# Kernel tuning notes

Measured on AMD Instinct MI355X. Metric: run time of the kernel, lower is better.

Reference implementation:

```python
import jax, jax.numpy as jnp
import numpy as np

N_FREQ = 256
VOCAB = 50257
N_CHANNELS = 1024
B, S = 4, 1024


def setup_inputs() -> dict:
    key = jax.random.key(0)
    k1, k2 = jax.random.split(key)
    h = jax.random.normal(k1, (B, S, N_CHANNELS), dtype=jnp.float32)
    weight = jax.random.normal(k2, (N_CHANNELS, 2 * N_FREQ), dtype=jnp.float32) * 0.02
    return {"h": h, "weight": weight}


def reference(h, weight):
    n = N_FREQ
    V = VOCAB
    # channel -> frequency coefficients (real part then imag part)
    Y_ri = h.astype(jnp.float32) @ weight  # [B, S, 2n]
    Y = jax.lax.complex(Y_ri[..., :n], Y_ri[..., n:])  # [B, S, n]
    # zero-padded half-spectrum: bins 1..n carry Y, DC and high bins are zero
    full = jnp.zeros(h.shape[:-1] + (V // 2 + 1,), dtype=jnp.complex64)
    full = full.at[..., 1:n + 1].set(Y)
    out = jnp.fft.irfft(full, n=V, axis=-1)  # [B, S, V]
    return out.astype(h.dtype)
```

## Files before the change

### kernel.cpp

```cpp
#include <hip/hip_runtime.h>
#include <hip/hip_fp16.h>
#include <stdint.h>

#define V_N   50257
#define NPAN  393
#define NCH   1024
#define MT    4096
#define KC    512
#define NFRQ  256
#define TWO_PI 6.28318530717958647692f

typedef _Float16 f16;
typedef __attribute__((ext_vector_type(8))) _Float16 f16x8;
typedef __attribute__((ext_vector_type(4))) float    f32x4;

__device__ __forceinline__ void gload_lds16(const void* g, const void* l) {
  typedef const __attribute__((address_space(1))) unsigned int* gp_t;
  typedef __attribute__((address_space(3))) unsigned int* lp_t;
  __builtin_amdgcn_global_load_lds((gp_t)(uint64_t)(uintptr_t)g,
                                   (lp_t)(uint32_t)(uintptr_t)l, 16, 0, 0);
}

__global__ __launch_bounds__(256) void k1_proj(
    const float* __restrict__ h, const float* __restrict__ w, f16* __restrict__ A) {
  __shared__ __align__(16) f16 As[64 * 64];
  __shared__ __align__(16) f16 Bs[64 * 64];
  const int tid = threadIdx.x;
  const int bn0 = blockIdx.x * 64;
  const int bm0 = blockIdx.y * 64;
  const int lane = tid & 63, wid = tid >> 6;
  const int lr = lane & 15, lg = lane >> 4;
  const int wr = wid >> 1, wc = wid & 1;

  f32x4 acc[2][2];
#pragma unroll
  for (int i = 0; i < 2; ++i)
#pragma unroll
    for (int j = 0; j < 2; ++j) acc[i][j] = (f32x4){0.f, 0.f, 0.f, 0.f};

  for (int s = 0; s < NCH / 64; ++s) {
    const int k0 = s * 64;
    __syncthreads();
#pragma unroll
    for (int r = 0; r < 2; ++r) {
      int q = tid + r * 256;
      int m = q >> 3, c = q & 7;
      const float* src = h + (size_t)(bm0 + m) * NCH + k0 + c * 8;
      f32x4 v0 = *(const f32x4*)src;
      f32x4 v1 = *(const f32x4*)(src + 4);
      f16x8 pk;
#pragma unroll
      for (int e = 0; e < 4; ++e) { pk[e] = (f16)v0[e]; pk[4 + e] = (f16)v1[e]; }
      *(f16x8*)&As[m * 64 + ((c ^ (m & 7)) << 3)] = pk;
    }
#pragma unroll
    for (int r = 0; r < 2; ++r) {
      int q = tid + r * 256;
      int c = q >> 6, n = q & 63;
      int jj = bn0 + n;
      int wcol = (jj >> 1) + ((jj & 1) ? NFRQ : 0);
      f16x8 pk;
#pragma unroll
      for (int j = 0; j < 8; ++j)
        pk[j] = (f16)w[(size_t)(k0 + c * 8 + j) * KC + wcol];
      *(f16x8*)&Bs[n * 64 + ((c ^ (n & 7)) << 3)] = pk;
    }
    __syncthreads();
#pragma unroll
    for (int kk = 0; kk < 2; ++kk) {
      const int cb = kk * 4 + lg;
      f16x8 a[2], b[2];
#pragma unroll
      for (int mi = 0; mi < 2; ++mi) {
        int row = wr * 32 + mi * 16 + lr;
        a[mi] = *(const f16x8*)&As[row * 64 + ((cb ^ (row & 7)) << 3)];
      }
#pragma unroll
      for (int ni = 0; ni < 2; ++ni) {
        int col = wc * 32 + ni * 16 + lr;
        b[ni] = *(const f16x8*)&Bs[col * 64 + ((cb ^ (col & 7)) << 3)];
      }
#pragma unroll
      for (int mi = 0; mi < 2; ++mi)
#pragma unroll
        for (int ni = 0; ni < 2; ++ni)
          acc[mi][ni] = __builtin_amdgcn_mfma_f32_16x16x32_f16(a[mi], b[ni], acc[mi][ni], 0, 0, 0);
    }
  }
#pragma unroll
  for (int mi = 0; mi < 2; ++mi)
#pragma unroll
    for (int ni = 0; ni < 2; ++ni)
#pragma unroll
      for (int r = 0; r < 4; ++r) {
        int row = bm0 + wr * 32 + mi * 16 + lg * 4 + r;
        int col = bn0 + wc * 32 + ni * 16 + lr;
        A[(size_t)row * KC + col] = (f16)acc[mi][ni][r];
      }
}


__device__ __forceinline__ void stage_tile(const f16* __restrict__ M, int grow0,
                                           int kt, f16* dst, int wid, int lane) {
#pragma unroll
  for (int i = 0; i < 4; ++i) {
    int idx = wid * 4 + i;
    int q = idx * 64 + lane;
    int m = q >> 3, c = q & 7;
    int cg = c ^ (m & 7);
    gload_lds16(M + (size_t)(grow0 + m) * KC + kt * 64 + cg * 8, dst + idx * 512);
  }
}

__device__ __forceinline__ void compute_tile(
    const f16* __restrict__ CA, const f16* __restrict__ CB,
    int wr, int wc, int lr, int lg, f32x4 acc[4][4]) {
#pragma unroll
  for (int kk = 0; kk < 2; ++kk) {
    const int cb = kk * 4 + lg;
    f16x8 a[4], b[4];
#pragma unroll
    for (int mi = 0; mi < 4; ++mi) {
      int row = wr * 64 + mi * 16 + lr;
      a[mi] = *(const f16x8*)&CA[row * 64 + ((cb ^ (row & 7)) << 3)];
    }
#pragma unroll
    for (int ni = 0; ni < 4; ++ni) {
      int col = wc * 64 + ni * 16 + lr;
      b[ni] = *(const f16x8*)&CB[col * 64 + ((cb ^ (col & 7)) << 3)];
    }
    __builtin_amdgcn_s_setprio(1);
#pragma unroll
    for (int mi = 0; mi < 4; ++mi)
#pragma unroll
      for (int ni = 0; ni < 4; ++ni)
        acc[mi][ni] = __builtin_amdgcn_mfma_f32_16x16x32_f16(a[mi], b[ni], acc[mi][ni], 0, 0, 0);
    __builtin_amdgcn_s_setprio(0);
  }
}

__device__ __forceinline__ void seed_base(int s, int g, int t, float& br, float& bi) {
  int fb = 32 * s + 16 * g;
  int m = (fb * t) % V_N;
  float sn, cs;
  __sincosf((TWO_PI / (float)V_N) * (float)m, &sn, &cs);
  br = cs; bi = sn;
}

__device__ __forceinline__ void gen_bt(const float Tr[16], const float Ti[16],
                                       float br, float bi, f16x8 bt[4]) {
#pragma unroll
  for (int u = 0; u < 4; ++u)
#pragma unroll
    for (int p = 0; p < 4; ++p) {
      const int j = 4 * u + p;
      float re = br * Tr[j] - bi * Ti[j];
      float im = br * Ti[j] + bi * Tr[j];
      bt[u][2 * p]     = (f16)re;
      bt[u][2 * p + 1] = (f16)(-im);
    }
}

__device__ __forceinline__ void store_bt(f16* Bs, int nloc, int g, const f16x8 bt[4]) {
#pragma unroll
  for (int u = 0; u < 4; ++u) {
    int c = 4 * g + u;
    *(f16x8*)&Bs[nloc * 64 + ((c ^ (nloc & 7)) << 3)] = bt[u];
  }
}

__global__ __launch_bounds__(256, 3) void k2_otf4(
    const f16* __restrict__ A, float* __restrict__ out) {
  __shared__ __align__(16) f16 As0[128 * 64], As1[128 * 64];
  __shared__ __align__(16) f16 Bs[128 * 64];
  const int tid = threadIdx.x;
  const int orig = blockIdx.x;
  const int wgid = (orig & 7) * 1572 + (orig >> 3);
  const int by = wgid / 393;
  const int bx = wgid - by * 393;
  const int bn0 = bx << 7;
  const int bm0 = by << 7;
  const int lane = tid & 63, wid = tid >> 6;
  const int lr = lane & 15, lg = lane >> 4;
  const int wr = wid >> 1, wc = wid & 1;

  const int nloc = tid & 127;
  const int g = tid >> 7;
  int t = bn0 + nloc;
  if (t >= V_N) t -= V_N;
  const float w0 = TWO_PI / (float)V_N;
  float Tr[16], Ti[16];
#pragma unroll
  for (int j = 0; j < 16; ++j) {
    int m = ((j + 1) * t) % V_N;
    float sn, cs;
    __sincosf(w0 * (float)m, &sn, &cs);
    Tr[j] = cs; Ti[j] = sn;
  }

  f32x4 acc[4][4];
#pragma unroll
  for (int i = 0; i < 4; ++i)
#pragma unroll
    for (int j = 0; j < 4; ++j) acc[i][j] = (f32x4){0.f, 0.f, 0.f, 0.f};

  {
    float br, bi;
    seed_base(0, g, t, br, bi);
    f16x8 bt[4];
    gen_bt(Tr, Ti, br, bi, bt);
    store_bt(Bs, nloc, g, bt);
  }
  stage_tile(A, bm0, 0, As0, wid, lane);

  f16x8 btn[4];
  for (int s = 0; s < 8; ++s) {
    const bool nxt = (s < 7);
    f16* Ac = (s & 1) ? As1 : As0;
    f16* An = (s & 1) ? As0 : As1;
    if (nxt) {
      stage_tile(A, bm0, s + 1, An, wid, lane);
      float br, bi;
      seed_base(s + 1, g, t, br, bi);
      gen_bt(Tr, Ti, br, bi, btn);
    }
    asm volatile("s_waitcnt lgkmcnt(0)" ::: "memory");
    if (nxt) asm volatile("s_waitcnt vmcnt(4)" ::: "memory");
    else     asm volatile("s_waitcnt vmcnt(0)" ::: "memory");
    __builtin_amdgcn_s_barrier();
    compute_tile(Ac, Bs, wr, wc, lr, lg, acc);
    asm volatile("" ::: "memory");
    __builtin_amdgcn_s_barrier();
    if (nxt) store_bt(Bs, nloc, g, btn);
  }

  const float scale = 2.0f / (float)V_N;
#pragma unroll
  for (int ni = 0; ni < 4; ++ni) {
    int col = bn0 + wc * 64 + ni * 16 + lr;
    if (col < V_N) {
#pragma unroll
      for (int mi = 0; mi < 4; ++mi)
#pragma unroll
        for (int r = 0; r < 4; ++r) {
          int row = bm0 + wr * 64 + mi * 16 + lg * 4 + r;
          out[(size_t)row * V_N + col] = acc[mi][ni][r] * scale;
        }
    }
  }
}

extern "C" void kernel_launch(void* const* d_in, const int* in_sizes, int n_in,
                              void* d_out, int out_size, void* d_ws, size_t ws_size,
                              hipStream_t stream) {
  const float* h = (const float*)d_in[0];
  const float* w = (const float*)d_in[1];
  float* out = (float*)d_out;
  f16* A = (f16*)d_ws;

  dim3 blk(256);
  hipLaunchKernelGGL(k1_proj, dim3(KC / 64, MT / 64), blk, 0, stream, h, w, A);
  hipLaunchKernelGGL(k2_otf4, dim3(NPAN * 32), blk, 0, stream, A, out);
}
```

Measured before the change: 372.9 us.

## Store projection output in MFMA fragment order and load A directly to registers

k1_proj now writes its f16 output in a layout that matches the MFMA operand fragments. That lets k2 read A straight from global memory into registers, double-buffered across K steps, and drop the LDS staging buffers for A and the async global-to-LDS loads. The K loop is fully unrolled through a macro and the occupancy hint drops from 3 to 2 waves per SIMD. This removes LDS traffic and LDS footprint for A, at the cost of more registers, lower occupancy, and redundant global reads of A across the two waves that share the same rows.

```diff
diff --git a/kernel.cpp b/kernel.cpp
--- a/kernel.cpp
+++ b/kernel.cpp
@@ -14,12 +14,7 @@
 typedef __attribute__((ext_vector_type(8))) _Float16 f16x8;
 typedef __attribute__((ext_vector_type(4))) float    f32x4;
 
-__device__ __forceinline__ void gload_lds16(const void* g, const void* l) {
-  typedef const __attribute__((address_space(1))) unsigned int* gp_t;
-  typedef __attribute__((address_space(3))) unsigned int* lp_t;
-  __builtin_amdgcn_global_load_lds((gp_t)(uint64_t)(uintptr_t)g,
-                                   (lp_t)(uint32_t)(uintptr_t)l, 16, 0, 0);
-}
+#define CFENCE asm volatile("" ::: "memory")
 
 __global__ __launch_bounds__(256) void k1_proj(
     const float* __restrict__ h, const float* __restrict__ w, f16* __restrict__ A) {
@@ -95,35 +90,34 @@
       for (int r = 0; r < 4; ++r) {
         int row = bm0 + wr * 32 + mi * 16 + lg * 4 + r;
         int col = bn0 + wc * 32 + ni * 16 + lr;
-        A[(size_t)row * KC + col] = (f16)acc[mi][ni][r];
+        int r16 = row >> 4, lrA = row & 15;
+        int kt = col >> 6, q = col & 63;
+        int ks = q >> 5, lgA = (q >> 3) & 3, e = q & 7;
+        size_t off = ((((size_t)r16 * 8 + kt) * 2 + ks) * 4 + lgA) * 128 + lrA * 8 + e;
+        A[off] = (f16)acc[mi][ni][r];
       }
 }
 
 
-__device__ __forceinline__ void stage_tile(const f16* __restrict__ M, int grow0,
-                                           int kt, f16* dst, int wid, int lane) {
-#pragma unroll
-  for (int i = 0; i < 4; ++i) {
-    int idx = wid * 4 + i;
-    int q = idx * 64 + lane;
-    int m = q >> 3, c = q & 7;
-    int cg = c ^ (m & 7);
-    gload_lds16(M + (size_t)(grow0 + m) * KC + kt * 64 + cg * 8, dst + idx * 512);
-  }
-}
-
-__device__ __forceinline__ void compute_tile(
-    const f16* __restrict__ CA, const f16* __restrict__ CB,
+__device__ __forceinline__ void load_a(const f16* __restrict__ A, int bm0, int wr,
+                                       int kt, int lane, f16x8 a[4][2]) {
+  const int r16b = (bm0 >> 4) + wr * 4;
+#pragma unroll
+  for (int mi = 0; mi < 4; ++mi)
+#pragma unroll
+    for (int ks = 0; ks < 2; ++ks) {
+      size_t off = (((size_t)(r16b + mi) * 8 + kt) * 2 + ks) * 512 + (size_t)lane * 8;
+      a[mi][ks] = *(const f16x8*)&A[off];
+    }
+}
+
+__device__ __forceinline__ void compute_reg(
+    const f16x8 a[4][2], const f16* __restrict__ CB,
     int wr, int wc, int lr, int lg, f32x4 acc[4][4]) {
 #pragma unroll
-  for (int kk = 0; kk < 2; ++kk) {
-    const int cb = kk * 4 + lg;
-    f16x8 a[4], b[4];
-#pragma unroll
-    for (int mi = 0; mi < 4; ++mi) {
-      int row = wr * 64 + mi * 16 + lr;
-      a[mi] = *(const f16x8*)&CA[row * 64 + ((cb ^ (row & 7)) << 3)];
-    }
+  for (int ks = 0; ks < 2; ++ks) {
+    const int cb = ks * 4 + lg;
+    f16x8 b[4];
 #pragma unroll
     for (int ni = 0; ni < 4; ++ni) {
       int col = wc * 64 + ni * 16 + lr;
@@ -134,7 +128,7 @@
     for (int mi = 0; mi < 4; ++mi)
 #pragma unroll
       for (int ni = 0; ni < 4; ++ni)
-        acc[mi][ni] = __builtin_amdgcn_mfma_f32_16x16x32_f16(a[mi], b[ni], acc[mi][ni], 0, 0, 0);
+        acc[mi][ni] = __builtin_amdgcn_mfma_f32_16x16x32_f16(a[mi][ks], b[ni], acc[mi][ni], 0, 0, 0);
     __builtin_amdgcn_s_setprio(0);
   }
 }
@@ -169,9 +163,26 @@
   }
 }
 
-__global__ __launch_bounds__(256, 3) void k2_otf4(
+#define K2_TILE(S, AC, AN)                                                \
+  do {                                                                    \
+    enum { s_ = (S) };                                                    \
+    if (s_ < 7) {                                                         \
+      load_a(A, bm0, wr, s_ + 1, lane, AN);                               \
+      float br_, bi_;                                                     \
+      seed_base(s_ + 1, g, t, br_, bi_);                                  \
+      gen_bt(Tr, Ti, br_, bi_, btn);                                      \
+    }                                                                     \
+    CFENCE;                                                               \
+    asm volatile("s_waitcnt lgkmcnt(0)" ::: "memory");                    \
+    __builtin_amdgcn_s_barrier();                                         \
+    compute_reg(AC, Bs, wr, wc, lr, lg, acc);                             \
+    CFENCE;                                                               \
+    __builtin_amdgcn_s_barrier();                                         \
+    if (s_ < 7) store_bt(Bs, nloc, g, btn);                               \
+  } while (0)
+
+__global__ __launch_bounds__(256, 2) void k2_areg(
     const f16* __restrict__ A, float* __restrict__ out) {
-  __shared__ __align__(16) f16 As0[128 * 64], As1[128 * 64];
   __shared__ __align__(16) f16 Bs[128 * 64];
   const int tid = threadIdx.x;
   const int orig = blockIdx.x;
@@ -211,28 +222,17 @@
     gen_bt(Tr, Ti, br, bi, bt);
     store_bt(Bs, nloc, g, bt);
   }
-  stage_tile(A, bm0, 0, As0, wid, lane);
-
-  f16x8 btn[4];
-  for (int s = 0; s < 8; ++s) {
-    const bool nxt = (s < 7);
-    f16* Ac = (s & 1) ? As1 : As0;
-    f16* An = (s & 1) ? As0 : As1;
-    if (nxt) {
-      stage_tile(A, bm0, s + 1, An, wid, lane);
-      float br, bi;
-      seed_base(s + 1, g, t, br, bi);
-      gen_bt(Tr, Ti, br, bi, btn);
-    }
-    asm volatile("s_waitcnt lgkmcnt(0)" ::: "memory");
-    if (nxt) asm volatile("s_waitcnt vmcnt(4)" ::: "memory");
-    else     asm volatile("s_waitcnt vmcnt(0)" ::: "memory");
-    __builtin_amdgcn_s_barrier();
-    compute_tile(Ac, Bs, wr, wc, lr, lg, acc);
-    asm volatile("" ::: "memory");
-    __builtin_amdgcn_s_barrier();
-    if (nxt) store_bt(Bs, nloc, g, btn);
-  }
+  f16x8 aA[4][2], aB[4][2], btn[4];
+  load_a(A, bm0, wr, 0, lane, aA);
+
+  K2_TILE(0, aA, aB);
+  K2_TILE(1, aB, aA);
+  K2_TILE(2, aA, aB);
+  K2_TILE(3, aB, aA);
+  K2_TILE(4, aA, aB);
+  K2_TILE(5, aB, aA);
+  K2_TILE(6, aA, aB);
+  K2_TILE(7, aB, aA);
 
   const float scale = 2.0f / (float)V_N;
 #pragma unroll
@@ -260,5 +260,5 @@
 
   dim3 blk(256);
   hipLaunchKernelGGL(k1_proj, dim3(KC / 64, MT / 64), blk, 0, stream, h, w, A);
-  hipLaunchKernelGGL(k2_otf4, dim3(NPAN * 32), blk, 0, stream, A, out);
-}
+  hipLaunchKernelGGL(k2_areg, dim3(NPAN * 32), blk, 0, stream, A, out);
+}
```

Result: slower. 386.4 us (+3.6%).

## Overlap 192-column compute tiles so each block stores cache-line-aligned 160-column spans

Applied to the files above, without the earlier changes.

The output GEMM block now computes 192 columns with 6 waves (384 threads) but writes only 160 of them. The written window is shifted per row by an offset chosen so stores line up with 128-byte boundaries despite the odd row stride of 50257 floats. Store loops are reordered to be row-major per lane. The aim is to cut partial-line and misaligned write traffic on the large fp32 output. The cost is roughly 20% redundant MFMA and twiddle work, plus a larger LDS B tile that could affect occupancy.

```diff
diff --git a/kernel.cpp b/kernel.cpp
--- a/kernel.cpp
+++ b/kernel.cpp
@@ -3,7 +3,9 @@
 #include <stdint.h>
 
 #define V_N   50257
-#define NPAN  393
+#define BN_OWN 160
+#define BN_CMP 192
+#define NPAN_O 315
 #define NCH   1024
 #define MT    4096
 #define KC    512
@@ -102,19 +104,21 @@
 
 __device__ __forceinline__ void stage_tile(const f16* __restrict__ M, int grow0,
                                            int kt, f16* dst, int wid, int lane) {
-#pragma unroll
-  for (int i = 0; i < 4; ++i) {
-    int idx = wid * 4 + i;
-    int q = idx * 64 + lane;
-    int m = q >> 3, c = q & 7;
-    int cg = c ^ (m & 7);
-    gload_lds16(M + (size_t)(grow0 + m) * KC + kt * 64 + cg * 8, dst + idx * 512);
+  if (wid < 4) {
+#pragma unroll
+    for (int i = 0; i < 4; ++i) {
+      int idx = wid * 4 + i;
+      int q = idx * 64 + lane;
+      int m = q >> 3, c = q & 7;
+      int cg = c ^ (m & 7);
+      gload_lds16(M + (size_t)(grow0 + m) * KC + kt * 64 + cg * 8, dst + idx * 512);
+    }
   }
 }
 
 __device__ __forceinline__ void compute_tile(
     const f16* __restrict__ CA, const f16* __restrict__ CB,
-    int wr, int wc, int lr, int lg, f32x4 acc[4][4]) {
+    int wr, int wn, int lr, int lg, f32x4 acc[4][4]) {
 #pragma unroll
   for (int kk = 0; kk < 2; ++kk) {
     const int cb = kk * 4 + lg;
@@ -126,7 +130,7 @@
     }
 #pragma unroll
     for (int ni = 0; ni < 4; ++ni) {
-      int col = wc * 64 + ni * 16 + lr;
+      int col = wn * 64 + ni * 16 + lr;
       b[ni] = *(const f16x8*)&CB[col * 64 + ((cb ^ (col & 7)) << 3)];
     }
     __builtin_amdgcn_s_setprio(1);
@@ -169,23 +173,23 @@
   }
 }
 
-__global__ __launch_bounds__(256, 3) void k2_otf4(
+__global__ __launch_bounds__(384, 3) void k2_own(
     const f16* __restrict__ A, float* __restrict__ out) {
   __shared__ __align__(16) f16 As0[128 * 64], As1[128 * 64];
-  __shared__ __align__(16) f16 Bs[128 * 64];
+  __shared__ __align__(16) f16 Bs[192 * 64];
   const int tid = threadIdx.x;
   const int orig = blockIdx.x;
-  const int wgid = (orig & 7) * 1572 + (orig >> 3);
-  const int by = wgid / 393;
-  const int bx = wgid - by * 393;
-  const int bn0 = bx << 7;
+  const int wgid = (orig & 7) * 1260 + (orig >> 3);
+  const int by = wgid / NPAN_O;
+  const int bx = wgid - by * NPAN_O;
+  const int bn0 = bx * BN_OWN;
   const int bm0 = by << 7;
   const int lane = tid & 63, wid = tid >> 6;
   const int lr = lane & 15, lg = lane >> 4;
-  const int wr = wid >> 1, wc = wid & 1;
-
-  const int nloc = tid & 127;
-  const int g = tid >> 7;
+  const int wr = wid / 3, wn = wid % 3;
+
+  const int nloc = (tid < 192) ? tid : tid - 192;
+  const int g = (tid < 192) ? 0 : 1;
   int t = bn0 + nloc;
   if (t >= V_N) t -= V_N;
   const float w0 = TWO_PI / (float)V_N;
@@ -228,7 +232,7 @@
     if (nxt) asm volatile("s_waitcnt vmcnt(4)" ::: "memory");
     else     asm volatile("s_waitcnt vmcnt(0)" ::: "memory");
     __builtin_amdgcn_s_barrier();
-    compute_tile(Ac, Bs, wr, wc, lr, lg, acc);
+    compute_tile(Ac, Bs, wr, wn, lr, lg, acc);
     asm volatile("" ::: "memory");
     __builtin_amdgcn_s_barrier();
     if (nxt) store_bt(Bs, nloc, g, btn);
@@ -236,18 +240,20 @@
 
   const float scale = 2.0f / (float)V_N;
 #pragma unroll
-  for (int ni = 0; ni < 4; ++ni) {
-    int col = bn0 + wc * 64 + ni * 16 + lr;
-    if (col < V_N) {
-#pragma unroll
-      for (int mi = 0; mi < 4; ++mi)
-#pragma unroll
-        for (int r = 0; r < 4; ++r) {
-          int row = bm0 + wr * 64 + mi * 16 + lg * 4 + r;
-          out[(size_t)row * V_N + col] = acc[mi][ni][r] * scale;
-        }
-    }
-  }
+  for (int mi = 0; mi < 4; ++mi)
+#pragma unroll
+    for (int r = 0; r < 4; ++r) {
+      int row = bm0 + wr * 64 + mi * 16 + lg * 4 + r;
+      int dlt = (15 * row) & 31;
+      float* orow = out + (size_t)row * V_N;
+#pragma unroll
+      for (int ni = 0; ni < 4; ++ni) {
+        int cc = wn * 64 + ni * 16 + lr;
+        int c = bn0 + cc;
+        bool own = (cc >= dlt || bx == 0) && (cc < BN_OWN + dlt) && (c < V_N);
+        if (own) orow[c] = acc[mi][ni][r] * scale;
+      }
+    }
 }
 
 extern "C" void kernel_launch(void* const* d_in, const int* in_sizes, int n_in,
@@ -258,7 +264,6 @@
   float* out = (float*)d_out;
   f16* A = (f16*)d_ws;
 
-  dim3 blk(256);
-  hipLaunchKernelGGL(k1_proj, dim3(KC / 64, MT / 64), blk, 0, stream, h, w, A);
-  hipLaunchKernelGGL(k2_otf4, dim3(NPAN * 32), blk, 0, stream, A, out);
-}
+  hipLaunchKernelGGL(k1_proj, dim3(KC / 64, MT / 64), dim3(256), 0, stream, h, w, A);
+  hipLaunchKernelGGL(k2_own, dim3(NPAN_O * 32), dim3(384), 0, stream, A, out);
+}
```

After: 583.8 us. +56.6%, slower.
